# Kernel optimization log

Measured on AMD Instinct MI355X. Metric: run time of the kernel, lower is better.

Reference implementation:

```python
import jax, jax.numpy as jnp
import numpy as np

NUM_NODES = 200000
FEAT_DIM = 128
MAX_DEG = 128
B = 512
NUM_SAMPLES = [25, 10]  # layer_infos[0].num_samples, layer_infos[1].num_samples
DIMS = [128, 128, 128]


def setup_inputs() -> dict:
    key = jax.random.key(0)
    ks = jax.random.split(key, 9)
    s = 0.05
    return {
        "features": jax.random.normal(ks[0], (NUM_NODES, FEAT_DIM), jnp.float32),
        "adj": jax.random.randint(ks[1], (NUM_NODES, MAX_DEG), 0, NUM_NODES, jnp.int64),
        "batch1": jax.random.randint(ks[2], (B,), 0, NUM_NODES, jnp.int64),
        "cols1": jax.random.randint(ks[3], (B, NUM_SAMPLES[1]), 0, MAX_DEG, jnp.int64),
        "cols2": jax.random.randint(ks[4], (B * NUM_SAMPLES[1], NUM_SAMPLES[0]), 0, MAX_DEG, jnp.int64),
        "w_self_0": jax.random.normal(ks[5], (DIMS[0], DIMS[1]), jnp.float32) * s,
        "w_neigh_0": jax.random.normal(ks[6], (DIMS[0], DIMS[1]), jnp.float32) * s,
        "w_self_1": jax.random.normal(ks[7], (2 * DIMS[1], DIMS[2]), jnp.float32) * s,
        "w_neigh_1": jax.random.normal(ks[8], (2 * DIMS[1], DIMS[2]), jnp.float32) * s,
    }


def _mean_agg(self_vecs, neigh_vecs, w_self, w_neigh, act):
    # MeanAggregator (concat=True, no bias): mean over neighbor axis, two GEMMs, concat
    neigh_means = jnp.mean(neigh_vecs, axis=1)
    out = jnp.concatenate([self_vecs @ w_self, neigh_means @ w_neigh], axis=1)
    return act(out)


def reference(features, adj, batch1, cols1, cols2, w_self_0, w_neigh_0, w_self_1, w_neigh_1):
    num_layers = 2
    # --- sample(): multi-hop uniform neighbor sampling via adjacency gathers ---
    # hop 1 uses layer_infos[1].num_samples = 10, hop 2 uses layer_infos[0].num_samples = 25
    n1 = jnp.take_along_axis(adj[batch1], cols1, axis=1).reshape(-1)        # [B*10]
    n2 = jnp.take_along_axis(adj[n1], cols2, axis=1).reshape(-1)            # [B*10*25]
    samples = [batch1, n1, n2]
    support_sizes = [1, NUM_SAMPLES[1], NUM_SAMPLES[1] * NUM_SAMPLES[0]]
    # --- aggregate(): gather features, then per-layer mean aggregation ---
    hidden = [features[s] for s in samples]
    weights = [(w_self_0, w_neigh_0), (w_self_1, w_neigh_1)]
    batch_size = batch1.shape[0]
    for layer in range(num_layers):
        w_s, w_n = weights[layer]
        act = (lambda x: x) if layer == num_layers - 1 else jax.nn.relu
        next_hidden = []
        for hop in range(num_layers - layer):
            n_neigh = NUM_SAMPLES[num_layers - hop - 1]
            dim = hidden[hop].shape[1]
            neigh = hidden[hop + 1].reshape(batch_size * support_sizes[hop], n_neigh, dim)
            next_hidden.append(_mean_agg(hidden[hop], neigh, w_s, w_n, act))
        hidden = next_hidden
    return hidden[0]  # [B, 2*DIMS[2]] (concat=True)
```

## Files before the change

kernel.cpp:

```cpp
#include <hip/hip_runtime.h>
#include <hip/hip_bf16.h>

typedef __bf16 bf16x8 __attribute__((ext_vector_type(8)));
typedef __attribute__((ext_vector_type(4))) float floatx4;

#define BATCH 512
#define S1 10
#define S2 25
#define NK1 (BATCH * S1)
#define NK2 (NK1 * S2)
#define MROWS (BATCH + NK1)

__device__ __forceinline__ ushort f2b(float x) {
    unsigned u = __builtin_bit_cast(unsigned, x);
    u += 0x7fffu + ((u >> 16) & 1u);
    return (ushort)(u >> 16);
}
__device__ __forceinline__ float b2f(ushort b) {
    unsigned u = ((unsigned)b) << 16;
    return __builtin_bit_cast(float, u);
}

__global__ void k_sample_pack(const int* __restrict__ adj,
                              const int* __restrict__ batch1,
                              const int* __restrict__ cols1,
                              const int* __restrict__ cols2,
                              const float* __restrict__ ws0, const float* __restrict__ wn0,
                              const float* __restrict__ ws1, const float* __restrict__ wn1,
                              int* __restrict__ n1, int* __restrict__ n2,
                              ushort* __restrict__ wpack) {
    __shared__ int sn1[S1];
    int bid = blockIdx.x, tid = threadIdx.x;
    if (bid < BATCH) {
        int bnode = batch1[bid];
        if (tid < S1) {
            int c = cols1[bid * S1 + tid];
            int v = adj[bnode * 128 + c];
            sn1[tid] = v;
            n1[bid * S1 + tid] = v;
        }
        __syncthreads();
        if (tid < S1 * S2) {
            int j = tid / S2, l = tid - j * S2;
            int k = bid * S1 + j;
            int c = cols2[k * S2 + l];
            n2[k * S2 + l] = adj[sn1[j] * 128 + c];
        }
    } else {
        int pg = (bid - BATCH) * 256 + tid;
        const float* src; int KS; int p;
        if (pg < 16384)      { src = ws0; KS = 4; p = pg; }
        else if (pg < 32768) { src = wn0; KS = 4; p = pg - 16384; }
        else if (pg < 65536) { src = ws1; KS = 8; p = pg - 32768; }
        else                 { src = wn1; KS = 8; p = pg - 65536; }
        int j = p & 7, l = (p >> 3) & 63, rest = p >> 9;
        int ks = rest % KS, nt = rest / KS;
        int k = ks * 32 + 8 * (l >> 4) + j;
        int n = nt * 16 + (l & 15);
        wpack[pg] = f2b(src[k * 128 + n]);
    }
}

__global__ void k_gather(const float* __restrict__ feat,
                         const int* __restrict__ batch1,
                         const int* __restrict__ n1, const int* __restrict__ n2,
                         ushort* __restrict__ xs, ushort* __restrict__ xn) {
    int k = blockIdx.x, t = threadIdx.x;
    const float2* f2 = (const float2*)feat;
    int row, selfidx; const int* nn; int cnt; float inv;
    if (k < NK1) { row = BATCH + k; selfidx = n1[k]; nn = n2 + k * S2; cnt = S2; inv = 1.f / S2; }
    else { int i = k - NK1; row = i; selfidx = batch1[i]; nn = n1 + i * S1; cnt = S1; inv = 1.f / S1; }
    float2 h = f2[(long long)selfidx * 64 + t];
    ((unsigned*)xs)[row * 64 + t] = (unsigned)f2b(h.x) | ((unsigned)f2b(h.y) << 16);
    float sx = 0.f, sy = 0.f;
    for (int l = 0; l < cnt; l++) {
        float2 v = f2[(long long)nn[l] * 64 + t];
        sx += v.x; sy += v.y;
    }
    ((unsigned*)xn)[row * 64 + t] = (unsigned)f2b(sx * inv) | ((unsigned)f2b(sy * inv) << 16);
}

__global__ __launch_bounds__(256) void k_gemm0(const ushort* __restrict__ xs,
                                               const ushort* __restrict__ xn,
                                               const ushort* __restrict__ wpack,
                                               ushort* __restrict__ H) {
    __shared__ __align__(16) ushort A2[2][64][136];
    int r0 = blockIdx.x * 64;
    int tid = threadIdx.x;
    for (int idx = tid; idx < 2048; idx += 256) {
        int buf = idx >> 10, row = (idx >> 4) & 63, seg = idx & 15;
        const uint4* src = (const uint4*)(buf ? xn : xs);
        uint4 v = src[(r0 + row) * 16 + seg];
        *(uint4*)&A2[buf][row][seg * 8] = v;
    }
    __syncthreads();
    int wave = tid >> 6, lane = tid & 63;
    int arow = wave * 16 + (lane & 15);
    int acol = 8 * (lane >> 4);
    bf16x8 afrag[2][4];
#pragma unroll
    for (int h = 0; h < 2; h++)
#pragma unroll
        for (int ks = 0; ks < 4; ks++)
            afrag[h][ks] = *(const bf16x8*)&A2[h][arow][ks * 32 + acol];
    int orow = r0 + wave * 16 + (lane >> 4) * 4;
    int ocol = lane & 15;
#pragma unroll
    for (int h = 0; h < 2; h++) {
        const bf16x8* wp = (const bf16x8*)(wpack + h * 16384);
#pragma unroll
        for (int nt = 0; nt < 8; nt++) {
            floatx4 acc = {0.f, 0.f, 0.f, 0.f};
#pragma unroll
            for (int ks = 0; ks < 4; ks++)
                acc = __builtin_amdgcn_mfma_f32_16x16x32_bf16(afrag[h][ks], wp[(nt * 4 + ks) * 64 + lane], acc, 0, 0, 0);
#pragma unroll
            for (int q = 0; q < 4; q++) {
                float v = acc[q] > 0.f ? acc[q] : 0.f;
                H[(orow + q) * 256 + h * 128 + nt * 16 + ocol] = f2b(v);
            }
        }
    }
}

__global__ __launch_bounds__(128) void k_gemm1(const ushort* __restrict__ H,
                                               const ushort* __restrict__ wpack,
                                               float* __restrict__ out) {
    __shared__ __align__(16) ushort A2[2][32][264];
    int i0 = blockIdx.x * 32;
    int tid = threadIdx.x;
    const uint4* H4 = (const uint4*)H;
    for (int idx = tid; idx < 1024; idx += 128) {
        int row = idx >> 5, seg = idx & 31;
        uint4 v = H4[(i0 + row) * 32 + seg];
        *(uint4*)&A2[0][row][seg * 8] = v;
    }
    for (int idx = tid; idx < 1024; idx += 128) {
        int row = idx >> 5, seg = idx & 31;
        float s[8] = {0, 0, 0, 0, 0, 0, 0, 0};
        int base = BATCH + (i0 + row) * S1;
        for (int j = 0; j < S1; j++) {
            uint4 v = H4[(base + j) * 32 + seg];
            unsigned u[4] = {v.x, v.y, v.z, v.w};
#pragma unroll
            for (int q = 0; q < 4; q++) {
                s[q * 2]     += b2f((ushort)(u[q] & 0xffffu));
                s[q * 2 + 1] += b2f((ushort)(u[q] >> 16));
            }
        }
        unsigned o[4];
#pragma unroll
        for (int q = 0; q < 4; q++)
            o[q] = (unsigned)f2b(s[q * 2] * 0.1f) | ((unsigned)f2b(s[q * 2 + 1] * 0.1f) << 16);
        uint4 ov = make_uint4(o[0], o[1], o[2], o[3]);
        *(uint4*)&A2[1][row][seg * 8] = ov;
    }
    __syncthreads();
    int wave = tid >> 6, lane = tid & 63;
    int arow = wave * 16 + (lane & 15);
    int acol = 8 * (lane >> 4);
    int orow = i0 + wave * 16 + (lane >> 4) * 4;
    int ocol = lane & 15;
#pragma unroll
    for (int h = 0; h < 2; h++) {
        bf16x8 a[8];
#pragma unroll
        for (int ks = 0; ks < 8; ks++)
            a[ks] = *(const bf16x8*)&A2[h][arow][ks * 32 + acol];
        const bf16x8* wp = (const bf16x8*)(wpack + 32768 + h * 32768);
#pragma unroll
        for (int nt = 0; nt < 8; nt++) {
            floatx4 acc = {0.f, 0.f, 0.f, 0.f};
#pragma unroll
            for (int ks = 0; ks < 8; ks++)
                acc = __builtin_amdgcn_mfma_f32_16x16x32_bf16(a[ks], wp[(nt * 8 + ks) * 64 + lane], acc, 0, 0, 0);
#pragma unroll
            for (int q = 0; q < 4; q++)
                out[(orow + q) * 256 + h * 128 + nt * 16 + ocol] = acc[q];
        }
    }
}

extern "C" void kernel_launch(void* const* d_in, const int* in_sizes, int n_in,
                              void* d_out, int out_size, void* d_ws, size_t ws_size,
                              hipStream_t stream) {
    const float* features = (const float*)d_in[0];
    const int*   adj      = (const int*)d_in[1];
    const int*   batch1   = (const int*)d_in[2];
    const int*   cols1    = (const int*)d_in[3];
    const int*   cols2    = (const int*)d_in[4];
    const float* ws0      = (const float*)d_in[5];
    const float* wn0      = (const float*)d_in[6];
    const float* ws1      = (const float*)d_in[7];
    const float* wn1      = (const float*)d_in[8];
    float* out = (float*)d_out;

    char* p = (char*)d_ws;
    int*    n1    = (int*)p;
    int*    n2    = (int*)(p + 20480);
    ushort* xs    = (ushort*)(p + 532480);
    ushort* xn    = (ushort*)(p + 1974272);
    ushort* H     = (ushort*)(p + 3416064);
    ushort* wpack = (ushort*)(p + 6299648);

    if (ws_size < (size_t)6496256) return;

    hipLaunchKernelGGL(k_sample_pack, dim3(896), dim3(256), 0, stream,
                       adj, batch1, cols1, cols2, ws0, wn0, ws1, wn1, n1, n2, wpack);
    hipLaunchKernelGGL(k_gather, dim3(MROWS), dim3(64), 0, stream,
                       features, batch1, n1, n2, xs, xn);
    hipLaunchKernelGGL(k_gemm0, dim3(MROWS / 64), dim3(256), 0, stream,
                       xs, xn, wpack, H);
    hipLaunchKernelGGL(k_gemm1, dim3(BATCH / 32), dim3(128), 0, stream,
                       H, wpack, out);
}
```

Before: 241.0 us.

## Fuse sampling, gather, and both aggregation GEMMs into one per-batch kernel

```diff
diff --git a/kernel.cpp b/kernel.cpp
--- a/kernel.cpp
+++ b/kernel.cpp
@@ -7,9 +7,6 @@
 #define BATCH 512
 #define S1 10
 #define S2 25
-#define NK1 (BATCH * S1)
-#define NK2 (NK1 * S2)
-#define MROWS (BATCH + NK1)
 
 __device__ __forceinline__ ushort f2b(float x) {
     unsigned u = __builtin_bit_cast(unsigned, x);
@@ -20,163 +17,122 @@
     unsigned u = ((unsigned)b) << 16;
     return __builtin_bit_cast(float, u);
 }
-
-__global__ void k_sample_pack(const int* __restrict__ adj,
-                              const int* __restrict__ batch1,
-                              const int* __restrict__ cols1,
-                              const int* __restrict__ cols2,
-                              const float* __restrict__ ws0, const float* __restrict__ wn0,
-                              const float* __restrict__ ws1, const float* __restrict__ wn1,
-                              int* __restrict__ n1, int* __restrict__ n2,
-                              ushort* __restrict__ wpack) {
-    __shared__ int sn1[S1];
-    int bid = blockIdx.x, tid = threadIdx.x;
-    if (bid < BATCH) {
-        int bnode = batch1[bid];
-        if (tid < S1) {
-            int c = cols1[bid * S1 + tid];
-            int v = adj[bnode * 128 + c];
-            sn1[tid] = v;
-            n1[bid * S1 + tid] = v;
-        }
-        __syncthreads();
-        if (tid < S1 * S2) {
-            int j = tid / S2, l = tid - j * S2;
-            int k = bid * S1 + j;
-            int c = cols2[k * S2 + l];
-            n2[k * S2 + l] = adj[sn1[j] * 128 + c];
-        }
-    } else {
-        int pg = (bid - BATCH) * 256 + tid;
-        const float* src; int KS; int p;
-        if (pg < 16384)      { src = ws0; KS = 4; p = pg; }
-        else if (pg < 32768) { src = wn0; KS = 4; p = pg - 16384; }
-        else if (pg < 65536) { src = ws1; KS = 8; p = pg - 32768; }
-        else                 { src = wn1; KS = 8; p = pg - 65536; }
-        int j = p & 7, l = (p >> 3) & 63, rest = p >> 9;
-        int ks = rest % KS, nt = rest / KS;
-        int k = ks * 32 + 8 * (l >> 4) + j;
-        int n = nt * 16 + (l & 15);
-        wpack[pg] = f2b(src[k * 128 + n]);
-    }
+__device__ __forceinline__ unsigned pk2(float a, float b) {
+    return (unsigned)f2b(a) | ((unsigned)f2b(b) << 16);
 }
 
-__global__ void k_gather(const float* __restrict__ feat,
-                         const int* __restrict__ batch1,
-                         const int* __restrict__ n1, const int* __restrict__ n2,
-                         ushort* __restrict__ xs, ushort* __restrict__ xn) {
-    int k = blockIdx.x, t = threadIdx.x;
-    const float2* f2 = (const float2*)feat;
-    int row, selfidx; const int* nn; int cnt; float inv;
-    if (k < NK1) { row = BATCH + k; selfidx = n1[k]; nn = n2 + k * S2; cnt = S2; inv = 1.f / S2; }
-    else { int i = k - NK1; row = i; selfidx = batch1[i]; nn = n1 + i * S1; cnt = S1; inv = 1.f / S1; }
-    float2 h = f2[(long long)selfidx * 64 + t];
-    ((unsigned*)xs)[row * 64 + t] = (unsigned)f2b(h.x) | ((unsigned)f2b(h.y) << 16);
-    float sx = 0.f, sy = 0.f;
-    for (int l = 0; l < cnt; l++) {
-        float2 v = f2[(long long)nn[l] * 64 + t];
-        sx += v.x; sy += v.y;
-    }
-    ((unsigned*)xn)[row * 64 + t] = (unsigned)f2b(sx * inv) | ((unsigned)f2b(sy * inv) << 16);
+__global__ void k_pack(const float* __restrict__ ws0, const float* __restrict__ wn0,
+                       const float* __restrict__ ws1, const float* __restrict__ wn1,
+                       ushort* __restrict__ wpack) {
+    int pg = blockIdx.x * 256 + threadIdx.x;
+    const float* src; int KS; int p;
+    if (pg < 16384)      { src = ws0; KS = 4; p = pg; }
+    else if (pg < 32768) { src = wn0; KS = 4; p = pg - 16384; }
+    else if (pg < 65536) { src = ws1; KS = 8; p = pg - 32768; }
+    else                 { src = wn1; KS = 8; p = pg - 65536; }
+    int j = p & 7, l = (p >> 3) & 63, rest = p >> 9;
+    int ks = rest % KS, nt = rest / KS;
+    int k = ks * 32 + 8 * (l >> 4) + j;
+    int n = nt * 16 + (l & 15);
+    wpack[pg] = f2b(src[k * 128 + n]);
 }
 
-__global__ __launch_bounds__(256) void k_gemm0(const ushort* __restrict__ xs,
-                                               const ushort* __restrict__ xn,
+__global__ __launch_bounds__(256) void k_fused(const float* __restrict__ feat,
+                                               const int* __restrict__ adj,
+                                               const int* __restrict__ batch1,
+                                               const int* __restrict__ cols1,
+                                               const int* __restrict__ cols2,
                                                const ushort* __restrict__ wpack,
-                                               ushort* __restrict__ H) {
-    __shared__ __align__(16) ushort A2[2][64][136];
-    int r0 = blockIdx.x * 64;
-    int tid = threadIdx.x;
-    for (int idx = tid; idx < 2048; idx += 256) {
-        int buf = idx >> 10, row = (idx >> 4) & 63, seg = idx & 15;
-        const uint4* src = (const uint4*)(buf ? xn : xs);
-        uint4 v = src[(r0 + row) * 16 + seg];
-        *(uint4*)&A2[buf][row][seg * 8] = v;
+                                               float* __restrict__ out) {
+    __shared__ int sn1[S1];
+    __shared__ int sn2[S1 * S2];
+    __shared__ __align__(16) ushort xs[16][136];
+    __shared__ __align__(16) ushort xn[16][136];
+    __shared__ __align__(16) ushort Hl[16][264];
+
+    int b = blockIdx.x, tid = threadIdx.x;
+    int wave = tid >> 6, lane = tid & 63;
+
+    if (tid < S1) {
+        int c = cols1[b * S1 + tid];
+        sn1[tid] = adj[batch1[b] * 128 + c];
     }
     __syncthreads();
-    int wave = tid >> 6, lane = tid & 63;
-    int arow = wave * 16 + (lane & 15);
-    int acol = 8 * (lane >> 4);
-    bf16x8 afrag[2][4];
-#pragma unroll
-    for (int h = 0; h < 2; h++)
+    if (tid < S1 * S2) {
+        int j = tid / S2, l = tid - j * S2;
+        sn2[tid] = adj[sn1[j] * 128 + cols2[(b * S1 + j) * S2 + l]];
+    }
+    __syncthreads();
+
+    {
+        const float2* f2p = (const float2*)feat;
+        for (int g = wave; g < 11; g += 4) {
+            int selfidx; const int* lst; int cnt; float inv;
+            if (g == 0) { selfidx = batch1[b]; lst = sn1; cnt = S1; inv = 1.f / S1; }
+            else        { selfidx = sn1[g - 1]; lst = sn2 + (g - 1) * S2; cnt = S2; inv = 1.f / S2; }
+            float2 h = f2p[(long long)selfidx * 64 + lane];
+            ((unsigned*)&xs[g][0])[lane] = pk2(h.x, h.y);
+            float sx = 0.f, sy = 0.f;
+            for (int l = 0; l < cnt; l++) {
+                float2 v = f2p[(long long)lst[l] * 64 + lane];
+                sx += v.x; sy += v.y;
+            }
+            ((unsigned*)&xn[g][0])[lane] = pk2(sx * inv, sy * inv);
+        }
+    }
+    __syncthreads();
+
+    {
+        int ntg0 = wave * 4;
+        const ushort (*At)[136] = (ntg0 < 8) ? xs : xn;
+        int arow = lane & 15, acol = 8 * (lane >> 4);
+        bf16x8 af[4];
 #pragma unroll
         for (int ks = 0; ks < 4; ks++)
-            afrag[h][ks] = *(const bf16x8*)&A2[h][arow][ks * 32 + acol];
-    int orow = r0 + wave * 16 + (lane >> 4) * 4;
-    int ocol = lane & 15;
+            af[ks] = *(const bf16x8*)&At[arow][ks * 32 + acol];
 #pragma unroll
-    for (int h = 0; h < 2; h++) {
-        const bf16x8* wp = (const bf16x8*)(wpack + h * 16384);
-#pragma unroll
-        for (int nt = 0; nt < 8; nt++) {
+        for (int t = 0; t < 4; t++) {
+            int ntg = ntg0 + t;
+            int half = ntg >> 3, ntl = ntg & 7;
+            const bf16x8* wp = (const bf16x8*)(wpack + half * 16384);
             floatx4 acc = {0.f, 0.f, 0.f, 0.f};
 #pragma unroll
             for (int ks = 0; ks < 4; ks++)
-                acc = __builtin_amdgcn_mfma_f32_16x16x32_bf16(afrag[h][ks], wp[(nt * 4 + ks) * 64 + lane], acc, 0, 0, 0);
+                acc = __builtin_amdgcn_mfma_f32_16x16x32_bf16(af[ks], wp[(ntl * 4 + ks) * 64 + lane], acc, 0, 0, 0);
+            int col = half * 128 + ntl * 16 + (lane & 15);
 #pragma unroll
             for (int q = 0; q < 4; q++) {
                 float v = acc[q] > 0.f ? acc[q] : 0.f;
-                H[(orow + q) * 256 + h * 128 + nt * 16 + ocol] = f2b(v);
+                Hl[(lane >> 4) * 4 + q][col] = f2b(v);
             }
         }
     }
-}
+    __syncthreads();
 
-__global__ __launch_bounds__(128) void k_gemm1(const ushort* __restrict__ H,
-                                               const ushort* __restrict__ wpack,
-                                               float* __restrict__ out) {
-    __shared__ __align__(16) ushort A2[2][32][264];
-    int i0 = blockIdx.x * 32;
-    int tid = threadIdx.x;
-    const uint4* H4 = (const uint4*)H;
-    for (int idx = tid; idx < 1024; idx += 128) {
-        int row = idx >> 5, seg = idx & 31;
-        uint4 v = H4[(i0 + row) * 32 + seg];
-        *(uint4*)&A2[0][row][seg * 8] = v;
-    }
-    for (int idx = tid; idx < 1024; idx += 128) {
-        int row = idx >> 5, seg = idx & 31;
-        float s[8] = {0, 0, 0, 0, 0, 0, 0, 0};
-        int base = BATCH + (i0 + row) * S1;
-        for (int j = 0; j < S1; j++) {
-            uint4 v = H4[(base + j) * 32 + seg];
-            unsigned u[4] = {v.x, v.y, v.z, v.w};
+    {
+        float s = 0.f;
 #pragma unroll
-            for (int q = 0; q < 4; q++) {
-                s[q * 2]     += b2f((ushort)(u[q] & 0xffffu));
-                s[q * 2 + 1] += b2f((ushort)(u[q] >> 16));
-            }
-        }
-        unsigned o[4];
-#pragma unroll
-        for (int q = 0; q < 4; q++)
-            o[q] = (unsigned)f2b(s[q * 2] * 0.1f) | ((unsigned)f2b(s[q * 2 + 1] * 0.1f) << 16);
-        uint4 ov = make_uint4(o[0], o[1], o[2], o[3]);
-        *(uint4*)&A2[1][row][seg * 8] = ov;
+        for (int j = 1; j <= S1; j++) s += b2f(Hl[j][tid]);
+        Hl[11][tid] = f2b(s * (1.f / S1));
     }
     __syncthreads();
-    int wave = tid >> 6, lane = tid & 63;
-    int arow = wave * 16 + (lane & 15);
-    int acol = 8 * (lane >> 4);
-    int orow = i0 + wave * 16 + (lane >> 4) * 4;
-    int ocol = lane & 15;
+
+    {
+        int ntg0 = wave * 4;
 #pragma unroll
-    for (int h = 0; h < 2; h++) {
-        bf16x8 a[8];
-#pragma unroll
-        for (int ks = 0; ks < 8; ks++)
-            a[ks] = *(const bf16x8*)&A2[h][arow][ks * 32 + acol];
-        const bf16x8* wp = (const bf16x8*)(wpack + 32768 + h * 32768);
-#pragma unroll
-        for (int nt = 0; nt < 8; nt++) {
+        for (int t = 0; t < 4; t++) {
+            int ntg = ntg0 + t;
+            int half = ntg >> 3, ntl = ntg & 7;
+            int srcrow = half ? 11 : 0;
+            const bf16x8* wp = (const bf16x8*)(wpack + 32768 + half * 32768);
             floatx4 acc = {0.f, 0.f, 0.f, 0.f};
 #pragma unroll
-            for (int ks = 0; ks < 8; ks++)
-                acc = __builtin_amdgcn_mfma_f32_16x16x32_bf16(a[ks], wp[(nt * 8 + ks) * 64 + lane], acc, 0, 0, 0);
-#pragma unroll
-            for (int q = 0; q < 4; q++)
-                out[(orow + q) * 256 + h * 128 + nt * 16 + ocol] = acc[q];
+            for (int ks = 0; ks < 8; ks++) {
+                bf16x8 a = *(const bf16x8*)&Hl[srcrow][ks * 32 + 8 * (lane >> 4)];
+                acc = __builtin_amdgcn_mfma_f32_16x16x32_bf16(a, wp[(ntl * 8 + ks) * 64 + lane], acc, 0, 0, 0);
+            }
+            if (lane < 16)
+                out[b * 256 + half * 128 + ntl * 16 + lane] = acc[0];
         }
     }
 }
@@ -195,22 +151,10 @@
     const float* wn1      = (const float*)d_in[8];
     float* out = (float*)d_out;
 
-    char* p = (char*)d_ws;
-    int*    n1    = (int*)p;
-    int*    n2    = (int*)(p + 20480);
-    ushort* xs    = (ushort*)(p + 532480);
-    ushort* xn    = (ushort*)(p + 1974272);
-    ushort* H     = (ushort*)(p + 3416064);
-    ushort* wpack = (ushort*)(p + 6299648);
+    ushort* wpack = (ushort*)d_ws;
+    if (ws_size < (size_t)196608) return;
 
-    if (ws_size < (size_t)6496256) return;
-
-    hipLaunchKernelGGL(k_sample_pack, dim3(896), dim3(256), 0, stream,
-                       adj, batch1, cols1, cols2, ws0, wn0, ws1, wn1, n1, n2, wpack);
-    hipLaunchKernelGGL(k_gather, dim3(MROWS), dim3(64), 0, stream,
-                       features, batch1, n1, n2, xs, xn);
-    hipLaunchKernelGGL(k_gemm0, dim3(MROWS / 64), dim3(256), 0, stream,
-                       xs, xn, wpack, H);
-    hipLaunchKernelGGL(k_gemm1, dim3(BATCH / 32), dim3(128), 0, stream,
-                       H, wpack, out);
+    hipLaunchKernelGGL(k_pack, dim3(384), dim3(256), 0, stream, ws0, wn0, ws1, wn1, wpack);
+    hipLaunchKernelGGL(k_fused, dim3(BATCH), dim3(256), 0, stream,
+                       features, adj, batch1, cols1, cols2, wpack, out);
 }
```

Measured after the change: 227.8 us. 1.06x faster.
